# Kernel optimization log

Hardware: AMD Instinct MI355X
Metric: run time of the kernel (lower is better)

The kernel has to match this reference:

```python
import jax, jax.numpy as jnp
import numpy as np

B, S, D = 2, 2048, 1024
H, DH = 16, 64
EPS = 1e-5

def setup_inputs() -> dict:
    key = jax.random.key(0)
    ks = jax.random.split(key, 8)
    s = 0.02
    return {
        "x": jax.random.normal(ks[0], (B, S, D), dtype=jnp.float32),
        "ln_gamma": jnp.ones((D,), jnp.float32),
        "ln_beta": jnp.zeros((D,), jnp.float32),
        "wq": jax.random.normal(ks[1], (D, H * DH), jnp.float32) * s,
        "bq": jnp.zeros((H * DH,), jnp.float32),
        "wk": jax.random.normal(ks[2], (D, H * DH), jnp.float32) * s,
        "bk": jnp.zeros((H * DH,), jnp.float32),
        "wv": jax.random.normal(ks[3], (D, H * DH), jnp.float32) * s,
        "bv": jnp.zeros((H * DH,), jnp.float32),
        "wo": jax.random.normal(ks[4], (H * DH, D), jnp.float32) * s,
        "bo": jnp.zeros((D,), jnp.float32),
    }

def reference(x, ln_gamma, ln_beta, wq, bq, wk, bk, wv, bv, wo, bo):
    # Pre-LayerNorm over d_model
    mu = jnp.mean(x, axis=-1, keepdims=True)
    var = jnp.var(x, axis=-1, keepdims=True)
    xn = (x - mu) * jax.lax.rsqrt(var + EPS) * ln_gamma + ln_beta

    b, s, _ = xn.shape
    q = (xn @ wq + bq).reshape(b, s, H, DH)
    k = (xn @ wk + bk).reshape(b, s, H, DH)
    v = (xn @ wv + bv).reshape(b, s, H, DH)

    scale = jnp.sqrt(jnp.float32(DH))
    scores = jnp.einsum('bihd,bjhd->bhij', q, k) / scale  # [b,h,s,s]
    att = jax.nn.softmax(scores, axis=-1)
    out = jnp.einsum('bhij,bjhd->bihd', att, v).reshape(b, s, H * DH)
    return out @ wo + bo
```

## Files before the change

### kernel.cpp

```cpp
#include <hip/hip_runtime.h>
#include <math.h>

#define SEQ   2048
#define DM    1024
#define NHEAD 16
#define HD    64
#define NTOK  4096
#define EPS   1e-5f
#define SCALE_C 0.18033688f

typedef __attribute__((ext_vector_type(8))) short v8s;
typedef __attribute__((ext_vector_type(4))) float v4f;
typedef unsigned short ushort_t;

#define GLOAD16(g, l) __builtin_amdgcn_global_load_lds( \
    (const __attribute__((address_space(1))) unsigned int*)(g), \
    (__attribute__((address_space(3))) unsigned int*)(l), 16, 0, 0)

__device__ __forceinline__ unsigned short f2bf(float f) {
  union { float f; unsigned u; } v; v.f = f;
  unsigned r = v.u + 0x7FFFu + ((v.u >> 16) & 1u);
  return (unsigned short)(r >> 16);
}

__device__ __forceinline__ unsigned pack2_bf16(float a, float b) {
  union { float f; unsigned u; } ua, ub;
  ua.f = a; ub.f = b;
  return __builtin_amdgcn_perm(ub.u + 0x8000u, ua.u + 0x8000u, 0x07060302u);
}

__global__ __launch_bounds__(256) void prep_kernel(
    const float* __restrict__ x, const float* __restrict__ g,
    const float* __restrict__ be, ushort_t* __restrict__ y,
    const float* __restrict__ w0, const float* __restrict__ w1,
    const float* __restrict__ w2, const float* __restrict__ w3,
    ushort_t* __restrict__ o0, ushort_t* __restrict__ o1,
    ushort_t* __restrict__ o2, ushort_t* __restrict__ o3) {
  __shared__ float tile[64][65];
  const int t = threadIdx.x;
  if (blockIdx.x < NTOK) {
    const int row = blockIdx.x;
    const float4 v = ((const float4*)(x + (size_t)row * DM))[t];
    float s  = v.x + v.y + v.z + v.w;
    float ss = v.x*v.x + v.y*v.y + v.z*v.z + v.w*v.w;
    #pragma unroll
    for (int off = 32; off > 0; off >>= 1) {
      s  += __shfl_down(s,  off, 64);
      ss += __shfl_down(ss, off, 64);
    }
    float* red = &tile[0][0];
    const int wid = t >> 6, lane = t & 63;
    if (lane == 0) { red[wid] = s; red[4 + wid] = ss; }
    __syncthreads();
    if (t == 0) {
      const float S  = red[0] + red[1] + red[2] + red[3];
      const float SS = red[4] + red[5] + red[6] + red[7];
      const float mu  = S * (1.0f / DM);
      const float var = SS * (1.0f / DM) - mu * mu;
      red[8] = mu; red[9] = rsqrtf(var + EPS);
    }
    __syncthreads();
    const float mu = red[8], r = red[9];
    const float4 gv = ((const float4*)g)[t];
    const float4 bv = ((const float4*)be)[t];
    ushort4 o;
    o.x = f2bf((v.x - mu) * r * gv.x + bv.x);
    o.y = f2bf((v.y - mu) * r * gv.y + bv.y);
    o.z = f2bf((v.z - mu) * r * gv.z + bv.z);
    o.w = f2bf((v.w - mu) * r * gv.w + bv.w);
    *(ushort4*)(y + (size_t)row * DM + t * 4) = o;
  } else {
    const int w = blockIdx.x - NTOK;
    const int z = w >> 8;
    const float* wp = (z==0) ? w0 : (z==1) ? w1 : (z==2) ? w2 : w3;
    ushort_t* o    = (z==0) ? o0 : (z==1) ? o1 : (z==2) ? o2 : o3;
    const int n0 = (w & 15) * 64, k0 = ((w >> 4) & 15) * 64;
    const int r = t >> 4, c4 = (t & 15) * 4;
    #pragma unroll
    for (int i = 0; i < 4; ++i) {
      const float4 v = *(const float4*)(wp + (size_t)(k0 + r + i*16) * DM + n0 + c4);
      tile[r + i*16][c4 + 0] = v.x;
      tile[r + i*16][c4 + 1] = v.y;
      tile[r + i*16][c4 + 2] = v.z;
      tile[r + i*16][c4 + 3] = v.w;
    }
    __syncthreads();
    #pragma unroll
    for (int i = 0; i < 4; ++i) {
      const int n = r + i*16;
      ushort4 o4;
      o4.x = f2bf(tile[c4 + 0][n]);
      o4.y = f2bf(tile[c4 + 1][n]);
      o4.z = f2bf(tile[c4 + 2][n]);
      o4.w = f2bf(tile[c4 + 3][n]);
      *(ushort4*)(o + (size_t)(n0 + n) * DM + k0 + c4) = o4;
    }
  }
}

__device__ __forceinline__ void gemm_main(ushort_t* lsa, ushort_t* lsb,
    const ushort_t* A, const ushort_t* WT, int m0, int n0, v4f acc[4][4]) {
  const int tid = threadIdx.x;
  const int wid = tid >> 6, lane = tid & 63;
  const int mh = (wid & 1) << 6, nh = (wid >> 1) << 6;
  const int r16 = lane & 15, quad = lane >> 4;
  const int srow = lane >> 2, sch = lane & 3;
  for (int k0 = 0; k0 < DM; k0 += 32) {
    __syncthreads();
    #pragma unroll
    for (int j = 0; j < 2; ++j) {
      const int o = wid * 2 + j;
      GLOAD16(A  + (size_t)(m0 + o*16 + srow) * DM + k0 + sch*8, lsa + o*512);
      GLOAD16(WT + (size_t)(n0 + o*16 + srow) * DM + k0 + sch*8, lsb + o*512);
    }
    __syncthreads();
    v8s af[4], bfr[4];
    #pragma unroll
    for (int i = 0; i < 4; ++i) {
      af[i]  = *(const v8s*)(lsa + (mh + i*16 + r16)*32 + quad*8);
      bfr[i] = *(const v8s*)(lsb + (nh + i*16 + r16)*32 + quad*8);
    }
    #pragma unroll
    for (int i = 0; i < 4; ++i)
      #pragma unroll
      for (int j = 0; j < 4; ++j)
        acc[i][j] = __builtin_amdgcn_mfma_f32_16x16x32_bf16(af[i], bfr[j], acc[i][j], 0, 0, 0);
  }
}

__global__ __launch_bounds__(256, 3) void gemm_qkv(const ushort_t* __restrict__ xn,
    const ushort_t* __restrict__ wtq, const ushort_t* __restrict__ wtk, const ushort_t* __restrict__ wtv,
    const float* __restrict__ bq, const float* __restrict__ bk, const float* __restrict__ bv,
    ushort_t* __restrict__ qo, ushort_t* __restrict__ ko, ushort_t* __restrict__ vto) {
  __shared__ ushort_t lsa[128*32];
  __shared__ ushort_t lsb[128*32];
  const int z = blockIdx.z;
  const ushort_t* WT = (z == 0) ? wtq : (z == 1) ? wtk : wtv;
  const float* bias  = (z == 0) ? bq  : (z == 1) ? bk  : bv;
  const int m0 = blockIdx.y * 128, n0 = blockIdx.x * 128;
  v4f acc[4][4];
  #pragma unroll
  for (int i = 0; i < 4; ++i)
    #pragma unroll
    for (int j = 0; j < 4; ++j) acc[i][j] = (v4f){0.f, 0.f, 0.f, 0.f};
  gemm_main(lsa, lsb, xn, WT, m0, n0, acc);
  const int tid = threadIdx.x, wid = tid >> 6, lane = tid & 63;
  const int mh = (wid & 1) << 6, nh = (wid >> 1) << 6;
  const int r16 = lane & 15, quad = lane >> 4;
  if (z < 2) {
    ushort_t* out = (z == 0) ? qo : ko;
    const float sc = (z == 0) ? SCALE_C : 1.0f;
    #pragma unroll
    for (int bn = 0; bn < 4; ++bn) {
      const int col = n0 + nh + bn*16 + r16;
      const float bb = bias[col];
      #pragma unroll
      for (int am = 0; am < 4; ++am) {
        const int tb = m0 + mh + am*16 + quad*4;
        #pragma unroll
        for (int r = 0; r < 4; ++r)
          out[(size_t)(tb + r) * DM + col] = f2bf((acc[am][bn][r] + bb) * sc);
      }
    }
  } else {
    #pragma unroll
    for (int bn = 0; bn < 4; ++bn) {
      const int col = n0 + nh + bn*16 + r16;
      const float bb = bias[col];
      const int h = col >> 6, d = col & 63;
      #pragma unroll
      for (int am = 0; am < 4; ++am) {
        const int tb = m0 + mh + am*16 + quad*4;
        const int b = tb >> 11, t = tb & 2047;
        ushort4 o4;
        o4.x = f2bf(acc[am][bn][0] + bb);
        o4.y = f2bf(acc[am][bn][1] + bb);
        o4.z = f2bf(acc[am][bn][2] + bb);
        o4.w = f2bf(acc[am][bn][3] + bb);
        *(ushort4*)(vto + ((size_t)(b*NHEAD + h) * HD + d) * SEQ + t) = o4;
      }
    }
  }
}

__global__ __launch_bounds__(256, 3) void gemm_out(const ushort_t* __restrict__ A,
    const ushort_t* __restrict__ WT, const float* __restrict__ bias,
    float* __restrict__ out) {
  __shared__ ushort_t lsa[128*32];
  __shared__ ushort_t lsb[128*32];
  const int m0 = blockIdx.y * 128, n0 = blockIdx.x * 128;
  v4f acc[4][4];
  #pragma unroll
  for (int i = 0; i < 4; ++i)
    #pragma unroll
    for (int j = 0; j < 4; ++j) acc[i][j] = (v4f){0.f, 0.f, 0.f, 0.f};
  gemm_main(lsa, lsb, A, WT, m0, n0, acc);
  const int tid = threadIdx.x, wid = tid >> 6, lane = tid & 63;
  const int mh = (wid & 1) << 6, nh = (wid >> 1) << 6;
  const int r16 = lane & 15, quad = lane >> 4;
  #pragma unroll
  for (int bn = 0; bn < 4; ++bn) {
    const int col = n0 + nh + bn*16 + r16;
    const float bb = bias[col];
    #pragma unroll
    for (int am = 0; am < 4; ++am) {
      const int tb = m0 + mh + am*16 + quad*4;
      #pragma unroll
      for (int r = 0; r < 4; ++r)
        out[(size_t)(tb + r) * DM + col] = acc[am][bn][r] + bb;
    }
  }
}

__global__ __launch_bounds__(256, 4) void attn_kernel(
    const ushort_t* __restrict__ Q, const ushort_t* __restrict__ K,
    const ushort_t* __restrict__ Vt, ushort_t* __restrict__ O) {
  __shared__ ushort_t kbuf[8*512];
  __shared__ ushort_t vbuf[8*512];
  __shared__ ushort_t pbuf[8*512];
  __shared__ float    lred[4][64];
  const int tid = threadIdx.x, wid = tid >> 6, lane = tid & 63;
  const int r16 = lane & 15, quad = lane >> 4;
  const int q0 = blockIdx.x * 64, bh = blockIdx.y;
  const int b = bh >> 4, h = bh & 15;
  const ushort_t* gQ = Q + (size_t)b * SEQ * DM + h * HD;
  const ushort_t* gK = K + (size_t)b * SEQ * DM + h * HD;
  const ushort_t* gV = Vt + (size_t)bh * HD * SEQ;

  v8s qfr[4][2];
  #pragma unroll
  for (int qa = 0; qa < 4; ++qa) {
    const ushort_t* p = gQ + (size_t)(q0 + qa*16 + r16) * DM + quad * 8;
    qfr[qa][0] = *(const v8s*)p;
    qfr[qa][1] = *(const v8s*)(p + 32);
  }
  v4f acco[4];
  #pragma unroll
  for (int i = 0; i < 4; ++i) acco[i] = (v4f){0.f, 0.f, 0.f, 0.f};
  float lrun[4] = {0.f, 0.f, 0.f, 0.f};

  const int pwoff = ((wid & 1) * 2 + (quad >> 1)) * 128 + r16 * 8 + (quad & 1) * 4;
  const int pblk0 = (wid >> 1) * 512;

  for (int kt = 0; kt < SEQ / 64; ++kt) {
    const int k0 = kt * 64;
    __syncthreads();
    if (wid < 2) {
      #pragma unroll
      for (int j = 0; j < 4; ++j) {
        const int o = (wid & 1) * 4 + j;
        GLOAD16(gK + (size_t)(k0 + (o >> 1) * 16 + r16) * DM + (o & 1) * 32 + quad * 8,
                kbuf + o * 512);
      }
    } else {
      #pragma unroll
      for (int j = 0; j < 4; ++j) {
        const int o = (wid & 1) * 4 + j;
        GLOAD16(gV + (size_t)((o & 3) * 16 + r16) * SEQ + k0 + (o >> 2) * 32 + quad * 8,
                vbuf + o * 512);
      }
    }
    __syncthreads();

    const v8s ka0 = *(const v8s*)(kbuf + (wid*2 + 0) * 512 + lane * 8);
    const v8s ka1 = *(const v8s*)(kbuf + (wid*2 + 1) * 512 + lane * 8);
    v4f sacc[4];
    #pragma unroll
    for (int qa = 0; qa < 4; ++qa) {
      sacc[qa] = (v4f){0.f, 0.f, 0.f, 0.f};
      sacc[qa] = __builtin_amdgcn_mfma_f32_16x16x32_bf16(ka0, qfr[qa][0], sacc[qa], 0, 0, 0);
      sacc[qa] = __builtin_amdgcn_mfma_f32_16x16x32_bf16(ka1, qfr[qa][1], sacc[qa], 0, 0, 0);
    }

    #pragma unroll
    for (int qa = 0; qa < 4; ++qa) {
      const float e0 = __builtin_amdgcn_exp2f(sacc[qa][0]);
      const float e1 = __builtin_amdgcn_exp2f(sacc[qa][1]);
      const float e2 = __builtin_amdgcn_exp2f(sacc[qa][2]);
      const float e3 = __builtin_amdgcn_exp2f(sacc[qa][3]);
      float ls = (e0 + e1) + (e2 + e3);
      ls += __shfl_xor(ls, 16, 64);
      ls += __shfl_xor(ls, 32, 64);
      lrun[qa] += ls;
      uint2 d2;
      d2.x = pack2_bf16(e0, e1);
      d2.y = pack2_bf16(e2, e3);
      *(uint2*)(pbuf + (qa*2) * 512 + pblk0 + pwoff) = d2;
    }

    __syncthreads();

    const v8s vf0 = *(const v8s*)(vbuf + (0*4 + wid) * 512 + lane * 8);
    const v8s vf1 = *(const v8s*)(vbuf + (1*4 + wid) * 512 + lane * 8);
    #pragma unroll
    for (int qa = 0; qa < 4; ++qa) {
      const v8s pb0 = *(const v8s*)(pbuf + (qa*2 + 0) * 512 + lane * 8);
      const v8s pb1 = *(const v8s*)(pbuf + (qa*2 + 1) * 512 + lane * 8);
      acco[qa] = __builtin_amdgcn_mfma_f32_16x16x32_bf16(vf0, pb0, acco[qa], 0, 0, 0);
      acco[qa] = __builtin_amdgcn_mfma_f32_16x16x32_bf16(vf1, pb1, acco[qa], 0, 0, 0);
    }
  }

  if (quad == 0) {
    #pragma unroll
    for (int qa = 0; qa < 4; ++qa) lred[wid][qa*16 + r16] = lrun[qa];
  }
  __syncthreads();
  ushort_t* gO = O + (size_t)b * SEQ * DM + h * HD;
  #pragma unroll
  for (int qa = 0; qa < 4; ++qa) {
    const int q = qa*16 + r16;
    const float inv = 1.f / ((lred[0][q] + lred[1][q]) + (lred[2][q] + lred[3][q]));
    ushort4 o4;
    o4.x = f2bf(acco[qa][0] * inv);
    o4.y = f2bf(acco[qa][1] * inv);
    o4.z = f2bf(acco[qa][2] * inv);
    o4.w = f2bf(acco[qa][3] * inv);
    *(ushort4*)(gO + (size_t)(q0 + q) * DM + wid*16 + quad*4) = o4;
  }
}

extern "C" void kernel_launch(void* const* d_in, const int* in_sizes, int n_in,
                              void* d_out, int out_size, void* d_ws, size_t ws_size,
                              hipStream_t stream) {
  const float* x     = (const float*)d_in[0];
  const float* gamma = (const float*)d_in[1];
  const float* beta  = (const float*)d_in[2];
  const float* wq    = (const float*)d_in[3];
  const float* bq    = (const float*)d_in[4];
  const float* wk    = (const float*)d_in[5];
  const float* bk    = (const float*)d_in[6];
  const float* wv    = (const float*)d_in[7];
  const float* bv    = (const float*)d_in[8];
  const float* wo    = (const float*)d_in[9];
  const float* bo    = (const float*)d_in[10];
  float* out = (float*)d_out;

  unsigned char* w8 = (unsigned char*)d_ws;
  const size_t MB = 1024 * 1024;
  ushort_t* xn  = (ushort_t*)(w8 + 0 * MB);
  ushort_t* qb  = (ushort_t*)(w8 + 8 * MB);
  ushort_t* kb  = (ushort_t*)(w8 + 16 * MB);
  ushort_t* vt  = (ushort_t*)(w8 + 24 * MB);
  ushort_t* wtq = (ushort_t*)(w8 + 32 * MB);
  ushort_t* wtk = (ushort_t*)(w8 + 34 * MB);
  ushort_t* wtv = (ushort_t*)(w8 + 36 * MB);
  ushort_t* wto = (ushort_t*)(w8 + 38 * MB);
  ushort_t* ob  = xn;

  prep_kernel<<<dim3(NTOK + 1024), dim3(256), 0, stream>>>(
      x, gamma, beta, xn, wq, wk, wv, wo, wtq, wtk, wtv, wto);
  gemm_qkv<<<dim3(8, 32, 3), dim3(256), 0, stream>>>(xn, wtq, wtk, wtv, bq, bk, bv, qb, kb, vt);
  attn_kernel<<<dim3(SEQ / 64, 2 * NHEAD), dim3(256), 0, stream>>>(qb, kb, vt, ob);
  gemm_out<<<dim3(8, 32, 1), dim3(256), 0, stream>>>(ob, wto, bo, out);
}
```

Before: 215.9 us.

## Load K/V fragments directly to registers with prefetch, double-buffer P

The attention kernel stops staging K and V tiles through LDS. Each wave now reads its own K and V MFMA fragments straight from global memory into registers and prefetches the next tile one iteration ahead. The P buffer is double-buffered, which cuts the per-iteration barriers from three to one. This removes LDS staging traffic and barrier stalls, at the cost of more VGPRs and global loads that are less coalesced and not shared across waves.

```diff
diff --git a/kernel.cpp b/kernel.cpp
--- a/kernel.cpp
+++ b/kernel.cpp
@@ -215,9 +215,7 @@
 __global__ __launch_bounds__(256, 4) void attn_kernel(
     const ushort_t* __restrict__ Q, const ushort_t* __restrict__ K,
     const ushort_t* __restrict__ Vt, ushort_t* __restrict__ O) {
-  __shared__ ushort_t kbuf[8*512];
-  __shared__ ushort_t vbuf[8*512];
-  __shared__ ushort_t pbuf[8*512];
+  __shared__ ushort_t pbuf[2][8*512];
   __shared__ float    lred[4][64];
   const int tid = threadIdx.x, wid = tid >> 6, lane = tid & 63;
   const int r16 = lane & 15, quad = lane >> 4;
@@ -239,39 +237,33 @@
   for (int i = 0; i < 4; ++i) acco[i] = (v4f){0.f, 0.f, 0.f, 0.f};
   float lrun[4] = {0.f, 0.f, 0.f, 0.f};
 
+  const ushort_t* kp = gK + (size_t)(wid*16 + r16) * DM + quad * 8;
+  const ushort_t* vp = gV + (size_t)(wid*16 + r16) * SEQ + quad * 8;
+
   const int pwoff = ((wid & 1) * 2 + (quad >> 1)) * 128 + r16 * 8 + (quad & 1) * 4;
   const int pblk0 = (wid >> 1) * 512;
 
+  v8s kc0 = *(const v8s*)kp, kc1 = *(const v8s*)(kp + 32);
+  v8s vc0 = *(const v8s*)vp, vc1 = *(const v8s*)(vp + 32);
+  kp += 64 * DM; vp += 64;
+
   for (int kt = 0; kt < SEQ / 64; ++kt) {
-    const int k0 = kt * 64;
-    __syncthreads();
-    if (wid < 2) {
-      #pragma unroll
-      for (int j = 0; j < 4; ++j) {
-        const int o = (wid & 1) * 4 + j;
-        GLOAD16(gK + (size_t)(k0 + (o >> 1) * 16 + r16) * DM + (o & 1) * 32 + quad * 8,
-                kbuf + o * 512);
-      }
-    } else {
-      #pragma unroll
-      for (int j = 0; j < 4; ++j) {
-        const int o = (wid & 1) * 4 + j;
-        GLOAD16(gV + (size_t)((o & 3) * 16 + r16) * SEQ + k0 + (o >> 2) * 32 + quad * 8,
-                vbuf + o * 512);
-      }
-    }
-    __syncthreads();
-
-    const v8s ka0 = *(const v8s*)(kbuf + (wid*2 + 0) * 512 + lane * 8);
-    const v8s ka1 = *(const v8s*)(kbuf + (wid*2 + 1) * 512 + lane * 8);
+    v8s kn0, kn1, vn0, vn1;
+    if (kt + 1 < SEQ / 64) {
+      kn0 = *(const v8s*)kp; kn1 = *(const v8s*)(kp + 32);
+      vn0 = *(const v8s*)vp; vn1 = *(const v8s*)(vp + 32);
+      kp += 64 * DM; vp += 64;
+    }
+
     v4f sacc[4];
     #pragma unroll
     for (int qa = 0; qa < 4; ++qa) {
       sacc[qa] = (v4f){0.f, 0.f, 0.f, 0.f};
-      sacc[qa] = __builtin_amdgcn_mfma_f32_16x16x32_bf16(ka0, qfr[qa][0], sacc[qa], 0, 0, 0);
-      sacc[qa] = __builtin_amdgcn_mfma_f32_16x16x32_bf16(ka1, qfr[qa][1], sacc[qa], 0, 0, 0);
-    }
-
+      sacc[qa] = __builtin_amdgcn_mfma_f32_16x16x32_bf16(kc0, qfr[qa][0], sacc[qa], 0, 0, 0);
+      sacc[qa] = __builtin_amdgcn_mfma_f32_16x16x32_bf16(kc1, qfr[qa][1], sacc[qa], 0, 0, 0);
+    }
+
+    ushort_t* pw = pbuf[kt & 1];
     #pragma unroll
     for (int qa = 0; qa < 4; ++qa) {
       const float e0 = __builtin_amdgcn_exp2f(sacc[qa][0]);
@@ -285,20 +277,20 @@
       uint2 d2;
       d2.x = pack2_bf16(e0, e1);
       d2.y = pack2_bf16(e2, e3);
-      *(uint2*)(pbuf + (qa*2) * 512 + pblk0 + pwoff) = d2;
-    }
-
-    __syncthreads();
-
-    const v8s vf0 = *(const v8s*)(vbuf + (0*4 + wid) * 512 + lane * 8);
-    const v8s vf1 = *(const v8s*)(vbuf + (1*4 + wid) * 512 + lane * 8);
+      *(uint2*)(pw + (qa*2) * 512 + pblk0 + pwoff) = d2;
+    }
+
+    __syncthreads();
+
     #pragma unroll
     for (int qa = 0; qa < 4; ++qa) {
-      const v8s pb0 = *(const v8s*)(pbuf + (qa*2 + 0) * 512 + lane * 8);
-      const v8s pb1 = *(const v8s*)(pbuf + (qa*2 + 1) * 512 + lane * 8);
-      acco[qa] = __builtin_amdgcn_mfma_f32_16x16x32_bf16(vf0, pb0, acco[qa], 0, 0, 0);
-      acco[qa] = __builtin_amdgcn_mfma_f32_16x16x32_bf16(vf1, pb1, acco[qa], 0, 0, 0);
-    }
+      const v8s pb0 = *(const v8s*)(pw + (qa*2 + 0) * 512 + lane * 8);
+      const v8s pb1 = *(const v8s*)(pw + (qa*2 + 1) * 512 + lane * 8);
+      acco[qa] = __builtin_amdgcn_mfma_f32_16x16x32_bf16(vc0, pb0, acco[qa], 0, 0, 0);
+      acco[qa] = __builtin_amdgcn_mfma_f32_16x16x32_bf16(vc1, pb1, acco[qa], 0, 0, 0);
+    }
+
+    kc0 = kn0; kc1 = kn1; vc0 = vn0; vc1 = vn1;
   }
 
   if (quad == 0) {
```

After: 216.1 us. No clear change (+0.1%).
